# Kernel optimization log

Measured on AMD Instinct MI355X. Metric: run time of the kernel, lower is better.

Reference implementation:

```python
import jax, jax.numpy as jnp
import numpy as np

HEADS = 4
OUT = 100   # = max_num_peds
IN = 100    # = max_num_peds
NEG_SLOPE = 0.2  # both GATConv attention leakyrelu (PyG default) and module's nn.LeakyReLU(0.2)


def setup_inputs() -> dict:
    key = jax.random.key(0)
    k0, k1, k2, k3 = jax.random.split(key, 4)
    A = jax.random.normal(k0, (1024, 100, 100), jnp.float32)
    # GATConv linear weight [heads*out, in] and attention vectors [heads, out]
    W = jax.random.normal(k1, (HEADS * OUT, IN), jnp.float32) * 0.1
    att_src = jax.random.normal(k2, (HEADS, OUT), jnp.float32) * 0.1
    att_dst = jax.random.normal(k3, (HEADS, OUT), jnp.float32) * 0.1
    bias = jnp.zeros((OUT,), jnp.float32)
    return {"A": A, "W": W, "att_src": att_src, "att_dst": att_dst, "bias": bias}


def reference(A, W, att_src, att_dst, bias):
    # A: [T, N, N] with N == max_num_peds, so the F.pad in the original is a no-op.
    T, _, N = A.shape
    X = jnp.swapaxes(A, 1, 2)                      # x = A_t.T for every t -> [T, N, IN]
    Wh = W.reshape(HEADS, OUT, IN)
    H = jnp.einsum('tnf,hof->tnho', X, Wh)         # per-head projected features [T,N,H,OUT]
    a_s = jnp.einsum('tnho,ho->tnh', H, att_src)   # source attention logits [T,N,H]
    a_d = jnp.einsum('tnho,ho->tnh', H, att_dst)   # dest attention logits   [T,N,H]
    # fully-connected graph + self loops (PyG add_self_loops=True) -> dense [T, i, j, H]
    logits = jax.nn.leaky_relu(a_d[:, :, None, :] + a_s[:, None, :, :], NEG_SLOPE)
    alpha = jax.nn.softmax(logits, axis=2)         # softmax over source nodes j per dest i
    out = jnp.einsum('tijh,tjho->tiho', alpha, H)  # aggregate [T,N,H,OUT]
    out = out.mean(axis=2) + bias                  # concat=False -> mean over heads, + bias
    x = jax.nn.leaky_relu(out, NEG_SLOPE)          # module's self.lrelu
    new_A = jnp.swapaxes(x, 1, 2)[:, :N, :N] + jnp.eye(N, dtype=A.dtype)
    return new_A
```

## Files before the change

kernel.cpp:

```cpp
#include <hip/hip_runtime.h>
#include <hip/hip_bf16.h>

typedef __attribute__((ext_vector_type(8))) short bf16x8;
typedef __attribute__((ext_vector_type(4))) float f32x4;
typedef __attribute__((ext_vector_type(4))) unsigned u32x4;

#define NEG 0.2f
#define CST 104
#define HSTRIDE 11648

__device__ __forceinline__ float lrelu(float x) { return x >= 0.0f ? x : NEG * x; }

__device__ __forceinline__ unsigned short f2bf(float x) {
    unsigned u = __builtin_bit_cast(unsigned, x);
    u += 0x7FFFu + ((u >> 16) & 1u);
    return (unsigned short)(u >> 16);
}
__device__ __forceinline__ unsigned pk2(float a, float b) {
    __hip_bfloat162 h = __float22bfloat162_rn(float2{a, b});
    unsigned r;
    __builtin_memcpy(&r, &h, sizeof(r));
    return r;
}
__device__ __forceinline__ float bflo(unsigned u) {
    unsigned v = u << 16; float f; __builtin_memcpy(&f, &v, 4); return f;
}
__device__ __forceinline__ float bfhi(unsigned u) {
    unsigned v = u & 0xffff0000u; float f; __builtin_memcpy(&f, &v, 4); return f;
}

extern "C" __global__ void prep_w(const float* __restrict__ W,
                                  const float* __restrict__ att_src,
                                  const float* __restrict__ att_dst,
                                  unsigned short* __restrict__ Wp)
{
    const int h = blockIdx.x;
    const int f = threadIdx.x;
    const float* __restrict__ Wh = W + h * 10000;
    unsigned short* __restrict__ D = Wp + h * HSTRIDE;
    float ws = 0.0f, wd = 0.0f;
    if (f < 100) {
        for (int o = 0; o < 100; ++o) {
            float wv = Wh[o * 100 + f];
            ws = fmaf(att_src[h * 100 + o], wv, ws);
            wd = fmaf(att_dst[h * 100 + o], wv, wd);
        }
    }
    if (f < CST) {
        for (int o = 0; o < 100; ++o)
            D[o * CST + f] = (f < 100) ? f2bf(Wh[o * 100 + f]) : (unsigned short)0;
        D[100 * CST + f] = (f < 100) ? f2bf(ws) : (unsigned short)0;
        D[101 * CST + f] = (f < 100) ? f2bf(wd) : (unsigned short)0;
        for (int o = 102; o < 112; ++o) D[o * CST + f] = 0;
    }
}

extern "C" __global__ void __launch_bounds__(512, 4)
gat16(const float* __restrict__ A, const unsigned short* __restrict__ Wp,
      const float* __restrict__ bias, float* __restrict__ out)
{
    extern __shared__ char smem[];
    unsigned short* P  = (unsigned short*)smem;
    unsigned short* HT = (unsigned short*)(smem + 23296);
    float* sas  = (float*)(smem + 46592);
    float* sad  = (float*)(smem + 47040);
    float* sOut = (float*)smem;

    const int t    = blockIdx.x;
    const int tid  = threadIdx.x;
    const int w    = tid >> 6;
    const int l    = tid & 63;
    const int lr   = l & 15;
    const int lk   = l >> 4;
    const bool HASW = (w < 7);
    const int row  = HASW ? w : 6;
    const int j0   = row * 16 + 4 * lk;
    const bool JW  = HASW && (j0 < 104);
    const float* __restrict__ At = A + (size_t)t * 10000u;
    const f32x4 z4 = {0, 0, 0, 0};

    for (int i = tid; i < 1456; i += 512) ((f32x4*)smem)[i] = z4;
    if (tid < 224) {
        float v = (tid >= 100 && tid < 112) ? -1e30f : 0.0f;
        ((float*)(smem + 46592))[tid] = v;
    }
    __syncthreads();

#pragma unroll
    for (int k = 0; k < 3; ++k) {
        const int q = tid + k * 512;
        if (q < 1250) {
            const int fp = q / 25, n0 = (q - fp * 25) * 4, f = fp * 2;
            float4 va = *(const float4*)(At + f * 100 + n0);
            float4 vb = *(const float4*)(At + (f + 1) * 100 + n0);
            *(unsigned*)(P + (n0 + 0) * CST + f) = pk2(va.x, vb.x);
            *(unsigned*)(P + (n0 + 1) * CST + f) = pk2(va.y, vb.y);
            *(unsigned*)(P + (n0 + 2) * CST + f) = pk2(va.z, vb.z);
            *(unsigned*)(P + (n0 + 3) * CST + f) = pk2(va.w, vb.w);
        }
    }
    __syncthreads();

    const bf16x8 zf = {0, 0, 0, 0, 0, 0, 0, 0};
    bf16x8 xf[4];
#pragma unroll
    for (int ks = 0; ks < 4; ++ks) {
        const bool kill = (ks == 3) && (lk != 0);
        const int koff = kill ? 96 : ks * 32 + lk * 8;
        bf16x8 v = *(const bf16x8*)(P + (row * 16 + lr) * CST + koff);
        xf[ks] = kill ? zf : v;
    }
    __syncthreads();

    f32x4 acc[7];
#pragma unroll
    for (int c = 0; c < 7; ++c) acc[c] = z4;

    for (int h = 0; h < 4; ++h) {
        {
            const u32x4* __restrict__ Wg = (const u32x4*)(Wp + h * HSTRIDE);
#pragma unroll
            for (int k = 0; k < 3; ++k) {
                const int q = tid + k * 512;
                if (q < 1456) ((u32x4*)P)[q] = Wg[q];
            }
        }
        __syncthreads();

#pragma unroll
        for (int half = 0; half < 2; ++half) {
            const int ntn = half ? 3 : 4;
            f32x4 c[4];
#pragma unroll
            for (int cc = 0; cc < 4; ++cc) c[cc] = z4;
#pragma unroll
            for (int ks = 0; ks < 4; ++ks) {
                const int koff = ks * 32 + lk * 8;
                bf16x8 b[4];
#pragma unroll
                for (int bb = 0; bb < 4; ++bb)
                    if (bb < ntn)
                        b[bb] = *(const bf16x8*)(P + ((half * 4 + bb) * 16 + lr) * CST + koff);
#pragma unroll
                for (int bb = 0; bb < 4; ++bb)
                    if (bb < ntn)
                        c[bb] = __builtin_amdgcn_mfma_f32_16x16x32_bf16(xf[ks], b[bb], c[bb], 0, 0, 0);
            }
#pragma unroll
            for (int bb = 0; bb < 4; ++bb)
                if (bb < ntn) {
                    const int o = (half * 4 + bb) * 16 + lr;
                    if (JW) {
                        uint2 pp;
                        pp.x = pk2(c[bb].x, c[bb].y);
                        pp.y = pk2(c[bb].z, c[bb].w);
                        *(uint2*)(HT + o * CST + j0) = pp;
                    }
                }
            if (half == 1) {
                if (lr == 4 && HASW && j0 < 100) *(f32x4*)(sas + j0) = c[2];
                if (lr == 5 && JW)               *(f32x4*)(sad + j0) = c[2];
            }
        }
        __syncthreads();

        const float adi = sad[row * 16 + lr];
        float sE = 0.0f;
        bf16x8 af[4];
#pragma unroll
        for (int ks = 0; ks < 4; ++ks) {
            const bool dead = (ks == 3) && (lk != 0);
            const int jb = dead ? 64 : ks * 32 + lk * 8;
            const f32x4 s0 = *(const f32x4*)(sas + jb);
            const f32x4 s1 = *(const f32x4*)(sas + jb + 4);
            float e0 = dead ? 0.0f : __expf(lrelu(adi + s0.x));
            float e1 = dead ? 0.0f : __expf(lrelu(adi + s0.y));
            float e2 = dead ? 0.0f : __expf(lrelu(adi + s0.z));
            float e3 = dead ? 0.0f : __expf(lrelu(adi + s0.w));
            float e4 = dead ? 0.0f : __expf(lrelu(adi + s1.x));
            float e5 = dead ? 0.0f : __expf(lrelu(adi + s1.y));
            float e6 = dead ? 0.0f : __expf(lrelu(adi + s1.z));
            float e7 = dead ? 0.0f : __expf(lrelu(adi + s1.w));
            sE += ((e0 + e1) + (e2 + e3)) + ((e4 + e5) + (e6 + e7));
            u32x4 uv;
            uv.x = pk2(e0, e1); uv.y = pk2(e2, e3);
            uv.z = pk2(e4, e5); uv.w = pk2(e6, e7);
            af[ks] = __builtin_bit_cast(bf16x8, uv);
        }
        sE += __shfl_xor(sE, 16);
        sE += __shfl_xor(sE, 32);
        const float invE = sE > 0.0f ? __builtin_amdgcn_rcpf(sE) : 0.0f;
#pragma unroll
        for (int ks = 0; ks < 4; ++ks) {
            u32x4 uv = __builtin_bit_cast(u32x4, af[ks]);
            uv.x = pk2(bflo(uv.x) * invE, bfhi(uv.x) * invE);
            uv.y = pk2(bflo(uv.y) * invE, bfhi(uv.y) * invE);
            uv.z = pk2(bflo(uv.z) * invE, bfhi(uv.z) * invE);
            uv.w = pk2(bflo(uv.w) * invE, bfhi(uv.w) * invE);
            af[ks] = __builtin_bit_cast(bf16x8, uv);
        }

#pragma unroll
        for (int half = 0; half < 2; ++half) {
            const int ntn = half ? 3 : 4;
#pragma unroll
            for (int ks = 0; ks < 4; ++ks) {
                const int koff = ks * 32 + lk * 8;
                bf16x8 b[4];
#pragma unroll
                for (int bb = 0; bb < 4; ++bb)
                    if (bb < ntn)
                        b[bb] = *(const bf16x8*)(HT + ((half * 4 + bb) * 16 + lr) * CST + koff);
#pragma unroll
                for (int bb = 0; bb < 4; ++bb)
                    if (bb < ntn)
                        acc[half * 4 + bb] = __builtin_amdgcn_mfma_f32_16x16x32_bf16(
                            af[ks], b[bb], acc[half * 4 + bb], 0, 0, 0);
            }
        }
    }
    __syncthreads();

    if (JW) {
        const int i0 = j0;
#pragma unroll
        for (int tn = 0; tn < 7; ++tn) {
            const int o = tn * 16 + lr;
            const float b = (o < 100) ? bias[o] : 0.0f;
            f32x4 v;
            v.x = lrelu(acc[tn].x * 0.25f + b) + ((i0 + 0) == o ? 1.0f : 0.0f);
            v.y = lrelu(acc[tn].y * 0.25f + b) + ((i0 + 1) == o ? 1.0f : 0.0f);
            v.z = lrelu(acc[tn].z * 0.25f + b) + ((i0 + 2) == o ? 1.0f : 0.0f);
            v.w = lrelu(acc[tn].w * 0.25f + b) + ((i0 + 3) == o ? 1.0f : 0.0f);
            *(f32x4*)(sOut + o * 104 + i0) = v;
        }
    }
    __syncthreads();

    float* __restrict__ outT = out + (size_t)t * 10000u;
    for (int q = tid; q < 2500; q += 512) {
        int o = q / 25, i0 = (q - o * 25) * 4;
        *(float4*)(outT + o * 100 + i0) = *(const float4*)(sOut + o * 104 + i0);
    }
}

extern "C" void kernel_launch(void* const* d_in, const int* in_sizes, int n_in,
                              void* d_out, int out_size, void* d_ws, size_t ws_size,
                              hipStream_t stream) {
    const float* A      = (const float*)d_in[0];
    const float* W      = (const float*)d_in[1];
    const float* attsrc = (const float*)d_in[2];
    const float* attdst = (const float*)d_in[3];
    const float* bias   = (const float*)d_in[4];
    float* outp = (float*)d_out;
    unsigned short* Wp = (unsigned short*)d_ws;

    const int T = in_sizes[0] / 10000;

    prep_w<<<4, 128, 0, stream>>>(W, attsrc, attdst, Wp);

    const int smem_bytes = 47488;
    gat16<<<T, 512, smem_bytes, stream>>>(A, Wp, bias, outp);
}
```

Baseline: 80.05 us.

## Load A fragments directly from global and parallelize weight prep kernel

The main kernel no longer stages the transposed A tile through shared memory. It drops the zero-fill loop and two barriers, and each lane gathers its bf16 MFMA fragment straight from global memory with strided scalar loads. The prep kernel now uses 512 threads, with a shared-memory reduction for the attention-projected weights and vectorized packed bf16 stores. The trade is that the per-lane global loads are uncoalesced, column-strided scalar reads, which could cost more than the shared-memory transpose they replace.

After: 68.14 us. 14.9% less time.

```diff
diff --git a/kernel.cpp b/kernel.cpp
--- a/kernel.cpp
+++ b/kernel.cpp
@@ -11,11 +11,6 @@
 
 __device__ __forceinline__ float lrelu(float x) { return x >= 0.0f ? x : NEG * x; }
 
-__device__ __forceinline__ unsigned short f2bf(float x) {
-    unsigned u = __builtin_bit_cast(unsigned, x);
-    u += 0x7FFFu + ((u >> 16) & 1u);
-    return (unsigned short)(u >> 16);
-}
 __device__ __forceinline__ unsigned pk2(float a, float b) {
     __hip_bfloat162 h = __float22bfloat162_rn(float2{a, b});
     unsigned r;
@@ -34,29 +29,52 @@
                                   const float* __restrict__ att_dst,
                                   unsigned short* __restrict__ Wp)
 {
-    const int h = blockIdx.x;
-    const int f = threadIdx.x;
+    __shared__ float red[2][4][128];
+    __shared__ float sWS[128], sWD[128];
+    const int h = blockIdx.x, tid = threadIdx.x;
+    const int f = tid & 127, og = tid >> 7;
     const float* __restrict__ Wh = W + h * 10000;
-    unsigned short* __restrict__ D = Wp + h * HSTRIDE;
     float ws = 0.0f, wd = 0.0f;
     if (f < 100) {
-        for (int o = 0; o < 100; ++o) {
+        for (int o = og * 25; o < og * 25 + 25; ++o) {
             float wv = Wh[o * 100 + f];
             ws = fmaf(att_src[h * 100 + o], wv, ws);
             wd = fmaf(att_dst[h * 100 + o], wv, wd);
         }
     }
-    if (f < CST) {
-        for (int o = 0; o < 100; ++o)
-            D[o * CST + f] = (f < 100) ? f2bf(Wh[o * 100 + f]) : (unsigned short)0;
-        D[100 * CST + f] = (f < 100) ? f2bf(ws) : (unsigned short)0;
-        D[101 * CST + f] = (f < 100) ? f2bf(wd) : (unsigned short)0;
-        for (int o = 102; o < 112; ++o) D[o * CST + f] = 0;
+    red[0][og][f] = ws;
+    red[1][og][f] = wd;
+    __syncthreads();
+    if (tid < 256) {
+        const int which = tid >> 7, ff = tid & 127;
+        float s = (red[which][0][ff] + red[which][1][ff]) +
+                  (red[which][2][ff] + red[which][3][ff]);
+        (which ? sWD : sWS)[ff] = s;
+    }
+    __syncthreads();
+    unsigned short* __restrict__ D = Wp + h * HSTRIDE;
+    for (int q = tid; q < 2912; q += 512) {
+        const int o = q / 26, f0 = (q - o * 26) * 4;
+        uint2 pp = {0u, 0u};
+        if (f0 < 100) {
+            if (o < 100) {
+                float4 wv = *(const float4*)(Wh + o * 100 + f0);
+                pp.x = pk2(wv.x, wv.y);
+                pp.y = pk2(wv.z, wv.w);
+            } else if (o == 100) {
+                pp.x = pk2(sWS[f0], sWS[f0 + 1]);
+                pp.y = pk2(sWS[f0 + 2], sWS[f0 + 3]);
+            } else if (o == 101) {
+                pp.x = pk2(sWD[f0], sWD[f0 + 1]);
+                pp.y = pk2(sWD[f0 + 2], sWD[f0 + 3]);
+            }
+        }
+        *(uint2*)(D + o * CST + f0) = pp;
     }
 }
 
 extern "C" __global__ void __launch_bounds__(512, 4)
-gat16(const float* __restrict__ A, const unsigned short* __restrict__ Wp,
+gat17(const float* __restrict__ A, const unsigned short* __restrict__ Wp,
       const float* __restrict__ bias, float* __restrict__ out)
 {
     extern __shared__ char smem[];
@@ -79,36 +97,30 @@
     const float* __restrict__ At = A + (size_t)t * 10000u;
     const f32x4 z4 = {0, 0, 0, 0};
 
-    for (int i = tid; i < 1456; i += 512) ((f32x4*)smem)[i] = z4;
     if (tid < 224) {
         float v = (tid >= 100 && tid < 112) ? -1e30f : 0.0f;
         ((float*)(smem + 46592))[tid] = v;
     }
-    __syncthreads();
-
-#pragma unroll
-    for (int k = 0; k < 3; ++k) {
-        const int q = tid + k * 512;
-        if (q < 1250) {
-            const int fp = q / 25, n0 = (q - fp * 25) * 4, f = fp * 2;
-            float4 va = *(const float4*)(At + f * 100 + n0);
-            float4 vb = *(const float4*)(At + (f + 1) * 100 + n0);
-            *(unsigned*)(P + (n0 + 0) * CST + f) = pk2(va.x, vb.x);
-            *(unsigned*)(P + (n0 + 1) * CST + f) = pk2(va.y, vb.y);
-            *(unsigned*)(P + (n0 + 2) * CST + f) = pk2(va.z, vb.z);
-            *(unsigned*)(P + (n0 + 3) * CST + f) = pk2(va.w, vb.w);
-        }
-    }
-    __syncthreads();
-
-    const bf16x8 zf = {0, 0, 0, 0, 0, 0, 0, 0};
+    if (tid >= 224 && tid < 240) ((unsigned*)(smem + 23296))[tid - 224] = 0;
+
+    const int col = row * 16 + lr;
+    const bool cOK = col < 100;
     bf16x8 xf[4];
 #pragma unroll
     for (int ks = 0; ks < 4; ++ks) {
         const bool kill = (ks == 3) && (lk != 0);
-        const int koff = kill ? 96 : ks * 32 + lk * 8;
-        bf16x8 v = *(const bf16x8*)(P + (row * 16 + lr) * CST + koff);
-        xf[ks] = kill ? zf : v;
+        const int koff = ks * 32 + lk * 8;
+        u32x4 uv = {0u, 0u, 0u, 0u};
+        if (cOK && !kill) {
+#pragma unroll
+            for (int jp = 0; jp < 4; ++jp) {
+                const int f0 = koff + jp * 2;
+                float a0 = (f0     < 100) ? At[f0 * 100 + col]       : 0.0f;
+                float a1 = (f0 + 1 < 100) ? At[(f0 + 1) * 100 + col] : 0.0f;
+                uv[jp] = pk2(a0, a1);
+            }
+        }
+        xf[ks] = __builtin_bit_cast(bf16x8, uv);
     }
     __syncthreads();
 
@@ -257,8 +269,8 @@
 
     const int T = in_sizes[0] / 10000;
 
-    prep_w<<<4, 128, 0, stream>>>(W, attsrc, attdst, Wp);
+    prep_w<<<4, 512, 0, stream>>>(W, attsrc, attdst, Wp);
 
     const int smem_bytes = 47488;
-    gat16<<<T, 512, smem_bytes, stream>>>(A, Wp, bias, outp);
-}
+    gat17<<<T, 512, smem_bytes, stream>>>(A, Wp, bias, outp);
+}
```
